# Performance work log

Hardware: AMD Instinct MI355X
Metric: run time of the kernel (lower is better)

## Reference

```python
import jax, jax.numpy as jnp
import numpy as np

NUM_HEADS = 6
KERNEL = 5
EPS = 1e-6


def _neighbor_idx(L, k):
    # NATTEN neighborhood: window start clamped so every query has exactly k neighbors
    starts = jnp.clip(jnp.arange(L) - k // 2, 0, L - k)
    return starts[:, None] + jnp.arange(k)  # [L, k]


def ada_rmsnorm(x, scale, w1, b1, w2, b2):
    # x: [B,C,D,H,W]; RMS over spatial dims, gamma from channel means via small MLP
    rms = jnp.sqrt(jnp.mean(x * x, axis=(2, 3, 4), keepdims=True) + EPS)
    xn = x / rms
    stats = jnp.mean(x, axis=(2, 3, 4))                 # [B,C]
    h = jax.nn.relu(stats @ w1.T + b1)                  # [B,2C]
    gamma = jax.nn.sigmoid(h @ w2.T + b2)               # [B,C]
    return xn * (scale * gamma[:, :, None, None, None])


def reference(x, scale1, n1_w1, n1_b1, n1_w2, n1_b2,
              qkv_w, qkv_b, proj_w, proj_b,
              scale2, n2_w1, n2_b1, n2_w2, n2_b2,
              mlp_w1, mlp_b1, mlp_w2, mlp_b2):
    B, C, D, H, W = x.shape
    nh_, k_ = NUM_HEADS, KERNEL
    hd = C // nh_
    K3 = k_ ** 3

    # --- norm1 + neighborhood attention ---
    h = ada_rmsnorm(x, scale1, n1_w1, n1_b1, n1_w2, n1_b2)
    t = jnp.transpose(h, (0, 2, 3, 4, 1))               # [B,D,H,W,C]
    qkv = t @ qkv_w.T + qkv_b                           # [B,D,H,W,3C]
    q, k, v = jnp.split(qkv, 3, axis=-1)
    q = q.reshape(B, D, H, W, nh_, hd)
    k = k.reshape(B, D, H, W, nh_, hd)
    v = v.reshape(B, D, H, W, nh_, hd)

    iD = _neighbor_idx(D, k_)
    iH = _neighbor_idx(H, k_)
    iW = _neighbor_idx(W, k_)
    nd = iD[:, None, None, :, None, None]               # [D,1,1,k,1,1]
    nhh = iH[None, :, None, None, :, None]              # [1,H,1,1,k,1]
    nw = iW[None, None, :, None, None, :]               # [1,1,W,1,1,k]

    k_nb = k[:, nd, nhh, nw].reshape(B, D, H, W, K3, nh_, hd)
    v_nb = v[:, nd, nhh, nw].reshape(B, D, H, W, K3, nh_, hd)

    scale_qk = hd ** -0.5
    scores = jnp.einsum('bdhwnc,bdhwknc->bdhwnk', q, k_nb) * scale_qk  # [B,D,H,W,heads,K3]
    p = jax.nn.softmax(scores, axis=-1)
    o = jnp.einsum('bdhwnk,bdhwknc->bdhwnc', p, v_nb).reshape(B, D, H, W, C)
    o = o @ proj_w.T + proj_b                            # output projection
    x = x + jnp.transpose(o, (0, 4, 1, 2, 3))

    # --- norm2 + 1x1-conv MLP (GELU exact) ---
    h2 = ada_rmsnorm(x, scale2, n2_w1, n2_b1, n2_w2, n2_b2)
    m = jnp.einsum('oc,bcdhw->bodhw', mlp_w1, h2) + mlp_b1[None, :, None, None, None]
    m = jax.nn.gelu(m, approximate=False)
    m = jnp.einsum('oc,bcdhw->bodhw', mlp_w2, m) + mlp_b2[None, :, None, None, None]
    return x + m


def setup_inputs() -> dict:
    key = jax.random.key(0)
    ks = jax.random.split(key, 16)
    B, C, D, H, W = 1, 192, 16, 16, 16
    hid = 2 * C
    mlp_h = int(4.0 * C)
    s = 0.02
    inp = {
        'x': jax.random.normal(ks[0], (B, C, D, H, W), jnp.float32),
        'scale1': jnp.ones((1, C, 1, 1, 1), jnp.float32),
        'n1_w1': jax.random.normal(ks[1], (hid, C), jnp.float32) * s,
        'n1_b1': jnp.zeros((hid,), jnp.float32),
        'n1_w2': jax.random.normal(ks[2], (C, hid), jnp.float32) * s,
        'n1_b2': jnp.zeros((C,), jnp.float32),
        'qkv_w': jax.random.normal(ks[3], (3 * C, C), jnp.float32) * s,
        'qkv_b': jnp.zeros((3 * C,), jnp.float32),
        'proj_w': jax.random.normal(ks[4], (C, C), jnp.float32) * s,
        'proj_b': jnp.zeros((C,), jnp.float32),
        'scale2': jnp.ones((1, C, 1, 1, 1), jnp.float32),
        'n2_w1': jax.random.normal(ks[5], (hid, C), jnp.float32) * s,
        'n2_b1': jnp.zeros((hid,), jnp.float32),
        'n2_w2': jax.random.normal(ks[6], (C, hid), jnp.float32) * s,
        'n2_b2': jnp.zeros((C,), jnp.float32),
        'mlp_w1': jax.random.normal(ks[7], (mlp_h, C), jnp.float32) * s,
        'mlp_b1': jnp.zeros((mlp_h,), jnp.float32),
        'mlp_w2': jax.random.normal(ks[8], (C, mlp_h), jnp.float32) * s,
        'mlp_b2': jnp.zeros((C,), jnp.float32),
    }
    return inp
```

## Files before the change

### kernel.cpp

```cpp
#include <hip/hip_runtime.h>
#include <hip/hip_bf16.h>
#include <cmath>


#define NPOS 4096
#define C_CH 192

typedef __bf16 bf16x8 __attribute__((ext_vector_type(8)));
typedef __bf16 bf16x4 __attribute__((ext_vector_type(4)));
typedef float  f32x4  __attribute__((ext_vector_type(4)));

__global__ __launch_bounds__(256) void prep_kernel(
    const float* __restrict__ s0, const float* __restrict__ s1,
    const float* __restrict__ s2, const float* __restrict__ s3,
    __bf16* __restrict__ d0, __bf16* __restrict__ d1,
    __bf16* __restrict__ d2, __bf16* __restrict__ d3,
    const float* __restrict__ x, float* __restrict__ sums, float* __restrict__ sumsq)
{
    int b = blockIdx.x;
    if (b < 432) {
        const float* src; __bf16* dst; int base;
        if (b < 108)      { src = s0; dst = d0; base = b; }
        else if (b < 144) { src = s1; dst = d1; base = b - 108; }
        else if (b < 288) { src = s2; dst = d2; base = b - 144; }
        else              { src = s3; dst = d3; base = b - 288; }
        int i = (base * 256 + threadIdx.x) * 4;
        float4 v = *(const float4*)(src + i);
        bf16x4 o = { (__bf16)v.x, (__bf16)v.y, (__bf16)v.z, (__bf16)v.w };
        *(bf16x4*)(dst + i) = o;
        return;
    }
    int c = b - 432;
    const float4* xc = (const float4*)(x + (size_t)c * NPOS);
    float a = 0.f, a2 = 0.f;
    for (int i = threadIdx.x; i < NPOS / 4; i += 256) {
        float4 v = xc[i];
        a  += v.x + v.y + v.z + v.w;
        a2 += v.x * v.x + v.y * v.y + v.z * v.z + v.w * v.w;
    }
    #pragma unroll
    for (int off = 32; off > 0; off >>= 1) {
        a  += __shfl_down(a, off);
        a2 += __shfl_down(a2, off);
    }
    __shared__ float ls[4], ls2[4];
    int wid = threadIdx.x >> 6;
    if ((threadIdx.x & 63) == 0) { ls[wid] = a; ls2[wid] = a2; }
    __syncthreads();
    if (threadIdx.x == 0) {
        float t = 0.f, t2 = 0.f;
        #pragma unroll
        for (int w = 0; w < 4; w++) { t += ls[w]; t2 += ls2[w]; }
        sums[c] = t; sumsq[c] = t2;
    }
}

__global__ __launch_bounds__(256) void stats_kernel(
    const float* __restrict__ x, float* __restrict__ sums, float* __restrict__ sumsq)
{
    int c = blockIdx.x;
    const float4* xc = (const float4*)(x + (size_t)c * NPOS);
    float a = 0.f, a2 = 0.f;
    for (int i = threadIdx.x; i < NPOS / 4; i += 256) {
        float4 v = xc[i];
        a  += v.x + v.y + v.z + v.w;
        a2 += v.x * v.x + v.y * v.y + v.z * v.z + v.w * v.w;
    }
    #pragma unroll
    for (int off = 32; off > 0; off >>= 1) {
        a  += __shfl_down(a, off);
        a2 += __shfl_down(a2, off);
    }
    __shared__ float ls[4], ls2[4];
    int wid = threadIdx.x >> 6;
    if ((threadIdx.x & 63) == 0) { ls[wid] = a; ls2[wid] = a2; }
    __syncthreads();
    if (threadIdx.x == 0) {
        float t = 0.f, t2 = 0.f;
        #pragma unroll
        for (int w = 0; w < 4; w++) { t += ls[w]; t2 += ls2[w]; }
        sums[c] = t; sumsq[c] = t2;
    }
}

__global__ __launch_bounds__(256) void convx_kernel(
    const float* __restrict__ x,
    const float* __restrict__ sums, const float* __restrict__ sumsq,
    const float* __restrict__ scale,
    const float* __restrict__ w1, const float* __restrict__ b1,
    const float* __restrict__ w2, const float* __restrict__ b2,
    __bf16* __restrict__ xb)
{
    __shared__ float stats[C_CH];
    __shared__ float h[384];
    __shared__ float gsl[C_CH];
    __shared__ float lds[192 * 17];
    int t = threadIdx.x;

    if (t < C_CH) stats[t] = sums[t] * (1.0f / (float)NPOS);
    __syncthreads();
    for (int j = t; j < 384; j += 256) {
        float acc = b1[j];
        const float* wr = w1 + (size_t)j * C_CH;
        #pragma unroll 4
        for (int c = 0; c < C_CH; c += 4) {
            float4 w4 = *(const float4*)(wr + c);
            acc += w4.x * stats[c] + w4.y * stats[c + 1] + w4.z * stats[c + 2] + w4.w * stats[c + 3];
        }
        h[j] = fmaxf(acc, 0.0f);
    }
    __syncthreads();
    if (t < C_CH) {
        float acc = b2[t];
        const float* wr = w2 + (size_t)t * 384;
        #pragma unroll 4
        for (int j = 0; j < 384; j += 4) {
            float4 w4 = *(const float4*)(wr + j);
            acc += w4.x * h[j] + w4.y * h[j + 1] + w4.z * h[j + 2] + w4.w * h[j + 3];
        }
        float g = 1.0f / (1.0f + __expf(-acc));
        float rms = sqrtf(sumsq[t] * (1.0f / (float)NPOS) + 1e-6f);
        gsl[t] = scale[t] * g / rms;
    }
    __syncthreads();

    int p0 = blockIdx.x * 16;
    for (int idx = t; idx < 192 * 4; idx += 256) {
        int row = idx >> 2, p4 = idx & 3;
        float4 v = *(const float4*)(x + (size_t)row * NPOS + p0 + p4 * 4);
        float g = gsl[row];
        lds[row * 17 + p4 * 4 + 0] = v.x * g;
        lds[row * 17 + p4 * 4 + 1] = v.y * g;
        lds[row * 17 + p4 * 4 + 2] = v.z * g;
        lds[row * 17 + p4 * 4 + 3] = v.w * g;
    }
    __syncthreads();
    for (int idx = t; idx < 48 * 16; idx += 256) {
        int c4 = idx >> 4, p = idx & 15;
        bf16x4 o;
        #pragma unroll
        for (int j = 0; j < 4; j++) o[j] = (__bf16)lds[(c4 * 4 + j) * 17 + p];
        *(bf16x4*)(xb + (size_t)(p0 + p) * 192 + c4 * 4) = o;
    }
}

template <int K, int EPI>
__global__ __launch_bounds__(256) void gemm_lds(
    const __bf16* __restrict__ W, const float* __restrict__ bias,
    const __bf16* __restrict__ X, void* __restrict__ out,
    const float* __restrict__ resid, int M,
    float* __restrict__ out_kv)
{
    constexpr int KC  = 192;
    constexpr int LDA = 200;
    __shared__ __bf16 al[64 * LDA];
    __shared__ __bf16 bl[64 * LDA];
    int t    = threadIdx.x;
    int lane = t & 63;
    int wv   = t >> 6;
    int r16  = lane & 15;
    int quad = lane >> 4;
    int wvm  = wv >> 1;
    int wvn  = wv & 1;
    int mBase = blockIdx.y * 64;
    int nBase = blockIdx.x * 64;

    f32x4 acc[2][2];
    #pragma unroll
    for (int i = 0; i < 2; i++)
        #pragma unroll
        for (int j = 0; j < 2; j++)
            acc[i][j] = (f32x4){0.f, 0.f, 0.f, 0.f};

    for (int k0 = 0; k0 < K; k0 += KC) {
        #pragma unroll
        for (int it = 0; it < 6; it++) {
            int c = it * 256 + t;
            int row = c / 24, off = c - row * 24;
            bf16x8 va = *(const bf16x8*)(W + (size_t)(mBase + row) * K + k0 + off * 8);
            *(bf16x8*)(al + row * LDA + off * 8) = va;
            bf16x8 vb = *(const bf16x8*)(X + (size_t)(nBase + row) * K + k0 + off * 8);
            *(bf16x8*)(bl + row * LDA + off * 8) = vb;
        }
        __syncthreads();
        #pragma unroll
        for (int ks = 0; ks < KC / 32; ks++) {
            bf16x8 a0 = *(const bf16x8*)(al + (wvm * 32 + r16) * LDA + ks * 32 + quad * 8);
            bf16x8 a1 = *(const bf16x8*)(al + (wvm * 32 + 16 + r16) * LDA + ks * 32 + quad * 8);
            bf16x8 b0 = *(const bf16x8*)(bl + (wvn * 32 + r16) * LDA + ks * 32 + quad * 8);
            bf16x8 b1 = *(const bf16x8*)(bl + (wvn * 32 + 16 + r16) * LDA + ks * 32 + quad * 8);
            acc[0][0] = __builtin_amdgcn_mfma_f32_16x16x32_bf16(a0, b0, acc[0][0], 0, 0, 0);
            acc[0][1] = __builtin_amdgcn_mfma_f32_16x16x32_bf16(a0, b1, acc[0][1], 0, 0, 0);
            acc[1][0] = __builtin_amdgcn_mfma_f32_16x16x32_bf16(a1, b0, acc[1][0], 0, 0, 0);
            acc[1][1] = __builtin_amdgcn_mfma_f32_16x16x32_bf16(a1, b1, acc[1][1], 0, 0, 0);
        }
        __syncthreads();
    }

    #pragma unroll
    for (int rt = 0; rt < 2; rt++) {
        int m0 = mBase + wvm * 32 + rt * 16 + quad * 4;
        float b0 = bias[m0], b1 = bias[m0 + 1], b2 = bias[m0 + 2], b3 = bias[m0 + 3];
        #pragma unroll
        for (int ct = 0; ct < 2; ct++) {
            int n = nBase + wvn * 32 + ct * 16 + r16;
            f32x4 a4 = acc[rt][ct];
            float g0 = a4[0] + b0, g1 = a4[1] + b1, g2 = a4[2] + b2, g3 = a4[3] + b3;
            if (EPI == 0) {
                int sect = m0 / 192;
                int o0 = m0 - sect * 192;
                if (sect == 0) {
                    const float qs = 0.17677669529663687f;
                    *(float4*)((float*)out + (size_t)n * 192 + o0) =
                        make_float4(g0 * qs, g1 * qs, g2 * qs, g3 * qs);
                } else {
                    *(float4*)(out_kv + (size_t)n * 384 + (sect - 1) * 192 + o0) =
                        make_float4(g0, g1, g2, g3);
                }
            } else if (EPI == 2) {
                float* o = (float*)out;
                size_t i0 = (size_t)m0 * NPOS + n;
                o[i0]            = g0 + resid[i0];
                o[i0 + NPOS]     = g1 + resid[i0 + NPOS];
                o[i0 + 2 * NPOS] = g2 + resid[i0 + 2 * NPOS];
                o[i0 + 3 * NPOS] = g3 + resid[i0 + 3 * NPOS];
            } else {
                bf16x4 v;
                v[0] = (__bf16)(0.5f * g0 * (1.0f + erff(g0 * 0.7071067811865475f)));
                v[1] = (__bf16)(0.5f * g1 * (1.0f + erff(g1 * 0.7071067811865475f)));
                v[2] = (__bf16)(0.5f * g2 * (1.0f + erff(g2 * 0.7071067811865475f)));
                v[3] = (__bf16)(0.5f * g3 * (1.0f + erff(g3 * 0.7071067811865475f)));
                *(bf16x4*)((__bf16*)out + (size_t)n * M + m0) = v;
            }
        }
    }
}

__global__ __launch_bounds__(256) void attn_kernel(
    const float* __restrict__ q, const float* __restrict__ kv, __bf16* __restrict__ o)
{
    int t = threadIdx.x;
    int pairIdx = blockIdx.x * 8 + (t >> 5);
    int sg   = (t >> 3) & 3;
    int lane = t & 7;
    int pos = pairIdx / 6;
    int head = pairIdx - pos * 6;
    int wq = pos & 15;
    int hq = (pos >> 4) & 15;
    int dq = pos >> 8;
    int d0 = min(max(dq - 2, 0), 11);
    int h0 = min(max(hq - 2, 0), 11);
    int w0 = min(max(wq - 2, 0), 11);

    const float* kvb = kv + head * 32 + lane * 4;
    float4 q4 = *(const float4*)(q + (size_t)pos * 192 + head * 32 + lane * 4);

    float l = 0.0f;
    float4 acc = make_float4(0.f, 0.f, 0.f, 0.f);

    for (int dh = sg; dh < 25; dh += 4) {
        int di = dh / 5;
        int hi = dh - di * 5;
        int np0 = (d0 + di) * 256 + (h0 + hi) * 16 + w0;
        const float* p = kvb + (size_t)np0 * 384;
        #pragma unroll
        for (int wi = 0; wi < 5; wi++) {
            float4 k4 = *(const float4*)p;
            float4 v4 = *(const float4*)(p + 192);
            float s = q4.x * k4.x + q4.y * k4.y + q4.z * k4.z + q4.w * k4.w;
            s += __shfl_xor(s, 1);
            s += __shfl_xor(s, 2);
            s += __shfl_xor(s, 4);
            float pr = __expf(s);
            l += pr;
            acc.x += pr * v4.x;
            acc.y += pr * v4.y;
            acc.z += pr * v4.z;
            acc.w += pr * v4.w;
            p += 384;
        }
    }

    #pragma unroll
    for (int off = 8; off <= 16; off <<= 1) {
        l     += __shfl_xor(l, off);
        acc.x += __shfl_xor(acc.x, off);
        acc.y += __shfl_xor(acc.y, off);
        acc.z += __shfl_xor(acc.z, off);
        acc.w += __shfl_xor(acc.w, off);
    }

    if (sg == 0) {
        float rl = 1.0f / l;
        bf16x4 ov = { (__bf16)(acc.x * rl), (__bf16)(acc.y * rl),
                      (__bf16)(acc.z * rl), (__bf16)(acc.w * rl) };
        *(bf16x4*)(o + (size_t)pos * 192 + head * 32 + lane * 4) = ov;
    }
}

extern "C" void kernel_launch(void* const* d_in, const int* in_sizes, int n_in,
                              void* d_out, int out_size, void* d_ws, size_t ws_size,
                              hipStream_t stream)
{
    const float* x      = (const float*)d_in[0];
    const float* scale1 = (const float*)d_in[1];
    const float* n1_w1  = (const float*)d_in[2];
    const float* n1_b1  = (const float*)d_in[3];
    const float* n1_w2  = (const float*)d_in[4];
    const float* n1_b2  = (const float*)d_in[5];
    const float* qkv_w  = (const float*)d_in[6];
    const float* qkv_b  = (const float*)d_in[7];
    const float* proj_w = (const float*)d_in[8];
    const float* proj_b = (const float*)d_in[9];
    const float* scale2 = (const float*)d_in[10];
    const float* n2_w1  = (const float*)d_in[11];
    const float* n2_b1  = (const float*)d_in[12];
    const float* n2_w2  = (const float*)d_in[13];
    const float* n2_b2  = (const float*)d_in[14];
    const float* mlp_w1 = (const float*)d_in[15];
    const float* mlp_b1 = (const float*)d_in[16];
    const float* mlp_w2 = (const float*)d_in[17];
    const float* mlp_b2 = (const float*)d_in[18];

    float* ws = (float*)d_ws;
    float*  q_buf  = ws;
    float*  kv_buf = ws + 786432;
    __bf16* m_buf  = (__bf16*)ws;
    __bf16* xb     = (__bf16*)(ws + 2359296);
    __bf16* o_attn = (__bf16*)(ws + 2752512);
    __bf16* qkv_wb = (__bf16*)(ws + 3145728);
    __bf16* proj_wb = qkv_wb + 110592;
    __bf16* m1_wb   = proj_wb + 36864;
    __bf16* m2_wb   = m1_wb + 147456;
    float*  sums   = ws + 3366912;
    float*  sumsq  = sums + 192;

    float* x2 = (float*)d_out;

    prep_kernel<<<624, 256, 0, stream>>>(qkv_w, proj_w, mlp_w1, mlp_w2,
                                         qkv_wb, proj_wb, m1_wb, m2_wb,
                                         x, sums, sumsq);
    convx_kernel<<<256, 256, 0, stream>>>(x, sums, sumsq, scale1,
                                          n1_w1, n1_b1, n1_w2, n1_b2, xb);
    gemm_lds<192, 0><<<dim3(64, 9), 256, 0, stream>>>(qkv_wb, qkv_b, xb, (void*)q_buf,
                                                      nullptr, 576, kv_buf);
    attn_kernel<<<3072, 256, 0, stream>>>(q_buf, kv_buf, o_attn);
    gemm_lds<192, 2><<<dim3(64, 3), 256, 0, stream>>>(proj_wb, proj_b, o_attn, (void*)x2,
                                                      x, 192, nullptr);
    stats_kernel<<<192, 256, 0, stream>>>(x2, sums, sumsq);
    convx_kernel<<<256, 256, 0, stream>>>(x2, sums, sumsq, scale2,
                                          n2_w1, n2_b1, n2_w2, n2_b2, xb);
    gemm_lds<192, 3><<<dim3(64, 12), 256, 0, stream>>>(m1_wb, mlp_b1, xb, (void*)m_buf,
                                                       nullptr, 768, nullptr);
    gemm_lds<768, 2><<<dim3(64, 3), 256, 0, stream>>>(m2_wb, mlp_b2, m_buf, (void*)x2,
                                                      x2, 192, nullptr);
}
```

Baseline: 200.1 us.

## Store K/V as interleaved bf16 and swizzle attention block order

The QKV GEMM epilogue now writes K and V as bf16, interleaving each 4-element K chunk with the matching V chunk, so the attention kernel fetches both with a single 16-byte load. This halves the K/V gather traffic and the number of load instructions in the neighborhood attention loop. The attention block index is also swizzled so consecutive blocks map to different spatial regions, which may change cache locality across compute units. Keys and values lose precision through bf16 rounding, and scores are still accumulated in fp32.

```diff
diff --git a/kernel.cpp b/kernel.cpp
--- a/kernel.cpp
+++ b/kernel.cpp
@@ -9,6 +9,13 @@
 typedef __bf16 bf16x8 __attribute__((ext_vector_type(8)));
 typedef __bf16 bf16x4 __attribute__((ext_vector_type(4)));
 typedef float  f32x4  __attribute__((ext_vector_type(4)));
+
+__device__ __forceinline__ float bflo(unsigned int u) {
+    union { unsigned int i; float f; } c; c.i = u << 16; return c.f;
+}
+__device__ __forceinline__ float bfhi(unsigned int u) {
+    union { unsigned int i; float f; } c; c.i = u & 0xffff0000u; return c.f;
+}
 
 __global__ __launch_bounds__(256) void prep_kernel(
     const float* __restrict__ s0, const float* __restrict__ s1,
@@ -149,7 +156,7 @@
     const __bf16* __restrict__ W, const float* __restrict__ bias,
     const __bf16* __restrict__ X, void* __restrict__ out,
     const float* __restrict__ resid, int M,
-    float* __restrict__ out_kv)
+    __bf16* __restrict__ out_kv)
 {
     constexpr int KC  = 192;
     constexpr int LDA = 200;
@@ -214,8 +221,8 @@
                     *(float4*)((float*)out + (size_t)n * 192 + o0) =
                         make_float4(g0 * qs, g1 * qs, g2 * qs, g3 * qs);
                 } else {
-                    *(float4*)(out_kv + (size_t)n * 384 + (sect - 1) * 192 + o0) =
-                        make_float4(g0, g1, g2, g3);
+                    bf16x4 kvv = { (__bf16)g0, (__bf16)g1, (__bf16)g2, (__bf16)g3 };
+                    *(bf16x4*)(out_kv + (size_t)n * 384 + (o0 >> 2) * 8 + (sect - 1) * 4) = kvv;
                 }
             } else if (EPI == 2) {
                 float* o = (float*)out;
@@ -237,10 +244,12 @@
 }
 
 __global__ __launch_bounds__(256) void attn_kernel(
-    const float* __restrict__ q, const float* __restrict__ kv, __bf16* __restrict__ o)
+    const float* __restrict__ q, const __bf16* __restrict__ kv, __bf16* __restrict__ o)
 {
     int t = threadIdx.x;
-    int pairIdx = blockIdx.x * 8 + (t >> 5);
+    int bid = blockIdx.x;
+    int swz = (bid & 7) * 384 + (bid >> 3);
+    int pairIdx = swz * 8 + (t >> 5);
     int sg   = (t >> 3) & 3;
     int lane = t & 7;
     int pos = pairIdx / 6;
@@ -252,7 +261,7 @@
     int h0 = min(max(hq - 2, 0), 11);
     int w0 = min(max(wq - 2, 0), 11);
 
-    const float* kvb = kv + head * 32 + lane * 4;
+    const __bf16* kvb = kv + head * 64 + lane * 8;
     float4 q4 = *(const float4*)(q + (size_t)pos * 192 + head * 32 + lane * 4);
 
     float l = 0.0f;
@@ -262,21 +271,21 @@
         int di = dh / 5;
         int hi = dh - di * 5;
         int np0 = (d0 + di) * 256 + (h0 + hi) * 16 + w0;
-        const float* p = kvb + (size_t)np0 * 384;
+        const __bf16* p = kvb + (size_t)np0 * 384;
         #pragma unroll
         for (int wi = 0; wi < 5; wi++) {
-            float4 k4 = *(const float4*)p;
-            float4 v4 = *(const float4*)(p + 192);
-            float s = q4.x * k4.x + q4.y * k4.y + q4.z * k4.z + q4.w * k4.w;
+            uint4 u = *(const uint4*)p;
+            float s = q4.x * bflo(u.x) + q4.y * bfhi(u.x)
+                    + q4.z * bflo(u.y) + q4.w * bfhi(u.y);
             s += __shfl_xor(s, 1);
             s += __shfl_xor(s, 2);
             s += __shfl_xor(s, 4);
             float pr = __expf(s);
             l += pr;
-            acc.x += pr * v4.x;
-            acc.y += pr * v4.y;
-            acc.z += pr * v4.z;
-            acc.w += pr * v4.w;
+            acc.x += pr * bflo(u.z);
+            acc.y += pr * bfhi(u.z);
+            acc.z += pr * bflo(u.w);
+            acc.w += pr * bfhi(u.w);
             p += 384;
         }
     }
@@ -324,7 +333,7 @@
 
     float* ws = (float*)d_ws;
     float*  q_buf  = ws;
-    float*  kv_buf = ws + 786432;
+    __bf16* kv_buf = (__bf16*)(ws + 786432);
     __bf16* m_buf  = (__bf16*)ws;
     __bf16* xb     = (__bf16*)(ws + 2359296);
     __bf16* o_attn = (__bf16*)(ws + 2752512);
```

Result: faster. 189.7 us (-5.2%).
